# Kernel optimization log

Hardware: AMD Instinct MI355X
Metric: run time of the kernel (lower is better)

Reference implementation:

```python
import jax, jax.numpy as jnp
import numpy as np

H = 1024      # hidden_size
L = 2         # num_layers
V = 32000     # src/tgt vocab
S = 512       # source length
T = 512       # target length
BOS = 0


def _gru_cell(h, x, Wih, Whh, bih, bhh):
    # h,x: [H]; Wih,Whh: [3H,H]; gate order r,z,n (PyTorch convention)
    gi = Wih @ x + bih
    gh = Whh @ h + bhh
    i_r, i_z, i_n = jnp.split(gi, 3)
    h_r, h_z, h_n = jnp.split(gh, 3)
    r = jax.nn.sigmoid(i_r + h_r)
    z = jax.nn.sigmoid(i_z + h_z)
    n = jnp.tanh(i_n + r * h_n)
    return (1.0 - z) * n + z * h


def _run_gru(xs, h0, Wih, Whh, bih, bhh):
    # xs: [T,H] embedded tokens; h0: [L,H]; weights: [L,3H,H]/[L,3H]
    n_layers = Wih.shape[0]

    def step(h, x):
        inp = x
        new_h = []
        for l in range(n_layers):  # small fixed layer loop
            hl = _gru_cell(h[l], inp, Wih[l], Whh[l], bih[l], bhh[l])
            new_h.append(hl)
            inp = hl
        return jnp.stack(new_h), inp  # carry [L,H], emit top-layer hidden

    return jax.lax.scan(step, h0, xs)


def setup_inputs() -> dict:
    key = jax.random.key(0)
    ks = jax.random.split(key, 16)
    sc = 1.0 / np.sqrt(H)

    def gw(k, shape):
        return (jax.random.normal(k, shape, dtype=jnp.float32) * sc)

    return {
        "src_tokens": jax.random.randint(ks[0], (S,), 0, V),
        "tgt_tokens": jax.random.randint(ks[1], (T,), 0, V),
        "src_emb": gw(ks[2], (V, H)),
        "tgt_emb": gw(ks[3], (V, H)),
        "enc_Wih": gw(ks[4], (L, 3 * H, H)),
        "enc_Whh": gw(ks[5], (L, 3 * H, H)),
        "enc_bih": gw(ks[6], (L, 3 * H)),
        "enc_bhh": gw(ks[7], (L, 3 * H)),
        "dec_Wih": gw(ks[8], (L, 3 * H, H)),
        "dec_Whh": gw(ks[9], (L, 3 * H, H)),
        "dec_bih": gw(ks[10], (L, 3 * H)),
        "dec_bhh": gw(ks[11], (L, 3 * H)),
        "out_W": gw(ks[12], (V, H)),
        "out_b": jnp.zeros((V,), dtype=jnp.float32),
    }


def reference(src_tokens, tgt_tokens, src_emb, tgt_emb,
              enc_Wih, enc_Whh, enc_bih, enc_bhh,
              dec_Wih, dec_Whh, dec_bih, dec_bhh,
              out_W, out_b):
    # ---- encoder: embed + L-layer GRU over source ----
    enc_x = src_emb[src_tokens]                       # [S,H]
    h0 = jnp.zeros((enc_Wih.shape[0], src_emb.shape[1]), src_emb.dtype)
    h_enc, _ = _run_gru(enc_x, h0, enc_Wih, enc_Whh, enc_bih, enc_bhh)
    # ---- decoder: teacher-forced inputs [BOS, tgt[:-1]] ----
    dec_in = jnp.concatenate(
        [jnp.array([BOS], dtype=tgt_tokens.dtype), tgt_tokens[:-1]])
    dec_x = tgt_emb[dec_in]                           # [T,H]
    _, dec_top = _run_gru(dec_x, h_enc, dec_Wih, dec_Whh, dec_bih, dec_bhh)
    logits = dec_top @ out_W.T + out_b                # [T,V]
    logp = jax.nn.log_softmax(logits, axis=-1)
    return logp[:, None, None, :]                     # [T,1,1,V] like torch.stack
```

## Files before the change

### kernel.cpp

```cpp
#include <hip/hip_runtime.h>
#include <hip/hip_bf16.h>
#include <math.h>


#define HID 1024
#define NSTEP 512
#define VOCAB 32000
#define SPIN_LIMIT 50000
typedef unsigned long long u64;

__device__ __forceinline__ u64 pack_hv(float v, unsigned tag) {
    return ((u64)tag << 32) | (u64)__float_as_uint(v);
}

__device__ __forceinline__ void poll16(const u64* __restrict__ row, unsigned want,
                                       float* v, int lane) {
    u64 p[16];
    int iter = 0;
    for (;;) {
        bool ok = true;
#pragma unroll
        for (int q = 0; q < 16; ++q) {
            p[q] = __hip_atomic_load((u64*)(row + q * 64 + lane),
                                     __ATOMIC_RELAXED, __HIP_MEMORY_SCOPE_AGENT);
            ok = ok && ((unsigned)(p[q] >> 32) == want);
        }
        if (ok) break;
        if (++iter >= SPIN_LIMIT) {
#pragma unroll
            for (int q = 0; q < 16; ++q) v[q] = __uint_as_float(0x7fc00000u);
            return;
        }
        __builtin_amdgcn_s_sleep(1);
    }
#pragma unroll
    for (int q = 0; q < 16; ++q)
        v[q] = __uint_as_float((unsigned)(p[q] & 0xffffffffu));
}

__global__ __launch_bounds__(256) void gather_embed(
    const int* __restrict__ src_tok, const int* __restrict__ tgt_tok,
    const float* __restrict__ src_emb, const float* __restrict__ tgt_emb,
    float* __restrict__ enc_x, float* __restrict__ dec_x) {
    int b = blockIdx.x, tid = threadIdx.x;
    int tok;
    const float* src;
    float* dst;
    if (b < 512) {
        tok = src_tok[b];
        src = src_emb;
        dst = enc_x + (size_t)b * HID;
    } else {
        int t = b - 512;
        tok = (t == 0) ? 0 : tgt_tok[t - 1];
        src = tgt_emb;
        dst = dec_x + (size_t)t * HID;
    }
    float4 v = *(const float4*)(src + (size_t)tok * HID + tid * 4);
    *(float4*)(dst + tid * 4) = v;
}

__global__ __launch_bounds__(256, 1) void gru_persist(
    const float* __restrict__ enc_x, const float* __restrict__ dec_x,
    const float* __restrict__ eWih, const float* __restrict__ eWhh,
    const float* __restrict__ eBih, const float* __restrict__ eBhh,
    const float* __restrict__ dWih, const float* __restrict__ dWhh,
    const float* __restrict__ dBih, const float* __restrict__ dBhh,
    u64* H0, u64* H1, u64* D0, u64* D1, float* __restrict__ D1f) {
    const int tid = threadIdx.x;
    const int wave = tid >> 6, lane = tid & 63;
    const int role = blockIdx.x >> 7;
    const int wl = blockIdx.x & 127;
    const int j0 = wl * 8;

    __shared__ float dots[48];
    __shared__ float sbias[48];

    float wreg[12][16];
    float hprev = 0.f;

#pragma unroll 1
    for (int phase = 0; phase < 2; ++phase) {
        const bool dec = (phase == 1);
        const float* Wih = (dec ? dWih : eWih) + (size_t)role * 3 * HID * HID;
        const float* Whh = (dec ? dWhh : eWhh) + (size_t)role * 3 * HID * HID;
        const float* bih = (dec ? dBih : eBih) + (size_t)role * 3 * HID;
        const float* bhh = (dec ? dBhh : eBhh) + (size_t)role * 3 * HID;
        u64* hch = dec ? (role ? D1 : D0) : (role ? H1 : H0);
        const unsigned tagOut = dec ? (role ? 4u : 3u) : (role ? 2u : 1u);
        const float* xf = dec ? dec_x : enc_x;
        const u64* xt = dec ? D0 : H0;
        const unsigned tagX = dec ? 3u : 1u;
        const u64* hinit = role ? (H1 + (size_t)(NSTEP - 1) * HID)
                                : (H0 + (size_t)(NSTEP - 1) * HID);
        const unsigned tagInit = role ? 2u : 1u;

        __syncthreads();
#pragma unroll
        for (int r = 0; r < 12; ++r) {
            int R = wave * 12 + r;
            int m = (R < 24) ? R : R - 24;
            const float* base = ((R < 24) ? Wih : Whh) +
                                (size_t)((m >> 3) * HID + j0 + (m & 7)) * HID;
#pragma unroll
            for (int q = 0; q < 16; ++q) wreg[r][q] = base[q * 64 + lane];
        }
        if (tid < 48) {
            int m = (tid < 24) ? tid : tid - 24;
            sbias[tid] = ((tid < 24) ? bih : bhh)[(m >> 3) * HID + j0 + (m & 7)];
        }
        __syncthreads();

#pragma unroll 1
        for (int t = 0; t < NSTEP; ++t) {
            float v[16];
            if (wave < 2) {
                if (role == 0) {
                    const float* xr = xf + (size_t)t * HID;
#pragma unroll
                    for (int q = 0; q < 16; ++q) v[q] = xr[q * 64 + lane];
                } else {
                    poll16(xt + (size_t)t * HID, tagX, v, lane);
                }
            } else {
                if (t > 0) {
                    poll16(hch + (size_t)(t - 1) * HID, tagOut, v, lane);
                } else if (dec) {
                    poll16(hinit, tagInit, v, lane);
                } else {
#pragma unroll
                    for (int q = 0; q < 16; ++q) v[q] = 0.f;
                }
            }

            float part[12];
#pragma unroll
            for (int r = 0; r < 12; ++r) {
                float a = 0.f;
#pragma unroll
                for (int q = 0; q < 16; ++q) a = fmaf(wreg[r][q], v[q], a);
                part[r] = a;
            }
#pragma unroll
            for (int off = 1; off < 64; off <<= 1) {
#pragma unroll
                for (int r = 0; r < 12; ++r) part[r] += __shfl_xor(part[r], off);
            }
            if (lane == 0) {
#pragma unroll
                for (int r = 0; r < 12; ++r) dots[wave * 12 + r] = part[r];
            }
            __syncthreads();

            if (tid < 8) {
                const int jj = tid;
                float ir = dots[jj] + sbias[jj];
                float iz = dots[8 + jj] + sbias[8 + jj];
                float in_ = dots[16 + jj] + sbias[16 + jj];
                float hr = dots[24 + jj] + sbias[24 + jj];
                float hz = dots[32 + jj] + sbias[32 + jj];
                float hn = dots[40 + jj] + sbias[40 + jj];
                float rg = 1.f / (1.f + __expf(-(ir + hr)));
                float zg = 1.f / (1.f + __expf(-(iz + hz)));
                float na = in_ + rg * hn;
                float ng = 2.f / (1.f + __expf(-2.f * na)) - 1.f;
                float hnew = (1.f - zg) * ng + zg * hprev;
                hprev = hnew;
                __hip_atomic_store((u64*)(hch + (size_t)t * HID + j0 + jj),
                                   pack_hv(hnew, tagOut),
                                   __ATOMIC_RELAXED, __HIP_MEMORY_SCOPE_AGENT);
                if (dec && role == 1) D1f[(size_t)t * HID + j0 + jj] = hnew;
            }
            __syncthreads();
        }
    }
}

__global__ __launch_bounds__(256) void gemm_out(
    const float* __restrict__ A, const float* __restrict__ B,
    const float* __restrict__ bias, float* __restrict__ C) {
    const int tid = threadIdx.x;
    const int bi = blockIdx.x;
    const int bv = blockIdx.y;
    const int i0 = bi * 64, v0 = bv * 128;
    __shared__ __align__(16) float As[32 * 68];
    __shared__ __align__(16) float Bs[32 * 132];
    const int tr = tid >> 4, tc = tid & 15;
    float c[4][8] = {};

    for (int kk = 0; kk < HID; kk += 32) {
#pragma unroll
        for (int q = 0; q < 2; q++) {
            int id = tid * 2 + q;
            int r = id >> 3, kq = id & 7;
            float4 a = *(const float4*)&A[(size_t)(i0 + r) * HID + kk + kq * 4];
            As[(kq * 4 + 0) * 68 + r] = a.x;
            As[(kq * 4 + 1) * 68 + r] = a.y;
            As[(kq * 4 + 2) * 68 + r] = a.z;
            As[(kq * 4 + 3) * 68 + r] = a.w;
        }
#pragma unroll
        for (int q = 0; q < 4; q++) {
            int id = tid * 4 + q;
            int vr = id >> 3, kq = id & 7;
            float4 b = *(const float4*)&B[(size_t)(v0 + vr) * HID + kk + kq * 4];
            Bs[(kq * 4 + 0) * 132 + vr] = b.x;
            Bs[(kq * 4 + 1) * 132 + vr] = b.y;
            Bs[(kq * 4 + 2) * 132 + vr] = b.z;
            Bs[(kq * 4 + 3) * 132 + vr] = b.w;
        }
        __syncthreads();
#pragma unroll
        for (int k = 0; k < 32; k++) {
            float4 a4 = *(const float4*)&As[k * 68 + tr * 4];
            float4 b0 = *(const float4*)&Bs[k * 132 + tc * 8];
            float4 b1 = *(const float4*)&Bs[k * 132 + tc * 8 + 4];
            float av[4] = {a4.x, a4.y, a4.z, a4.w};
            float bvv[8] = {b0.x, b0.y, b0.z, b0.w, b1.x, b1.y, b1.z, b1.w};
#pragma unroll
            for (int u = 0; u < 4; u++)
#pragma unroll
                for (int w = 0; w < 8; w++) c[u][w] += av[u] * bvv[w];
        }
        __syncthreads();
    }
    float4 bb0 = *(const float4*)&bias[v0 + tc * 8];
    float4 bb1 = *(const float4*)&bias[v0 + tc * 8 + 4];
#pragma unroll
    for (int u = 0; u < 4; u++) {
        int i = i0 + tr * 4 + u;
        float4 o0 = {c[u][0] + bb0.x, c[u][1] + bb0.y, c[u][2] + bb0.z, c[u][3] + bb0.w};
        float4 o1 = {c[u][4] + bb1.x, c[u][5] + bb1.y, c[u][6] + bb1.z, c[u][7] + bb1.w};
        *(float4*)&C[(size_t)i * VOCAB + v0 + tc * 8] = o0;
        *(float4*)&C[(size_t)i * VOCAB + v0 + tc * 8 + 4] = o1;
    }
}

__global__ __launch_bounds__(256) void log_softmax_inplace(float* __restrict__ C) {
    const int row = blockIdx.x;
    const int tid = threadIdx.x;
    float* p = C + (size_t)row * VOCAB;
    float m = -3.4e38f, s = 0.f;
    for (int idx = tid; idx < VOCAB / 4; idx += 256) {
        float4 x = ((const float4*)p)[idx];
        float xv[4] = {x.x, x.y, x.z, x.w};
#pragma unroll
        for (int u = 0; u < 4; u++) {
            float nm = fmaxf(m, xv[u]);
            s = s * __expf(m - nm) + __expf(xv[u] - nm);
            m = nm;
        }
    }
#pragma unroll
    for (int off = 1; off < 64; off <<= 1) {
        float om = __shfl_xor(m, off);
        float os = __shfl_xor(s, off);
        float nm = fmaxf(m, om);
        s = s * __expf(m - nm) + os * __expf(om - nm);
        m = nm;
    }
    __shared__ float sm[4], ss[4], sL;
    int wv = tid >> 6;
    if ((tid & 63) == 0) { sm[wv] = m; ss[wv] = s; }
    __syncthreads();
    if (tid == 0) {
        float M = sm[0], S = ss[0];
        for (int w = 1; w < 4; w++) {
            float nm = fmaxf(M, sm[w]);
            S = S * __expf(M - nm) + ss[w] * __expf(sm[w] - nm);
            M = nm;
        }
        sL = M + logf(S);
    }
    __syncthreads();
    float L = sL;
    for (int idx = tid; idx < VOCAB / 4; idx += 256) {
        float4 x = ((const float4*)p)[idx];
        x.x -= L; x.y -= L; x.z -= L; x.w -= L;
        ((float4*)p)[idx] = x;
    }
}

extern "C" void kernel_launch(void* const* d_in, const int* in_sizes, int n_in,
                              void* d_out, int out_size, void* d_ws, size_t ws_size,
                              hipStream_t stream) {
    const int* src_tok = (const int*)d_in[0];
    const int* tgt_tok = (const int*)d_in[1];
    const float* src_emb = (const float*)d_in[2];
    const float* tgt_emb = (const float*)d_in[3];
    const float* eWih = (const float*)d_in[4];
    const float* eWhh = (const float*)d_in[5];
    const float* eBih = (const float*)d_in[6];
    const float* eBhh = (const float*)d_in[7];
    const float* dWih = (const float*)d_in[8];
    const float* dWhh = (const float*)d_in[9];
    const float* dBih = (const float*)d_in[10];
    const float* dBhh = (const float*)d_in[11];
    const float* out_W = (const float*)d_in[12];
    const float* out_b = (const float*)d_in[13];
    float* out = (float*)d_out;

    char* ws = (char*)d_ws;
    float* enc_x = (float*)(ws);
    float* dec_x = (float*)(ws + (2ull << 20));
    u64* H0 = (u64*)(ws + (4ull << 20));
    u64* H1 = (u64*)(ws + (8ull << 20));
    u64* D0 = (u64*)(ws + (12ull << 20));
    u64* D1 = (u64*)(ws + (16ull << 20));
    float* D1f = (float*)(ws + (20ull << 20));

    hipMemsetAsync(ws + (4ull << 20), 0, 16ull << 20, stream);

    gather_embed<<<1024, 256, 0, stream>>>(src_tok, tgt_tok, src_emb, tgt_emb, enc_x, dec_x);
    gru_persist<<<256, 256, 0, stream>>>(enc_x, dec_x, eWih, eWhh, eBih, eBhh,
                                         dWih, dWhh, dBih, dBhh, H0, H1, D0, D1, D1f);
    gemm_out<<<dim3(8, 250), 256, 0, stream>>>(D1f, out_W, out_b, out);
    log_softmax_inplace<<<512, 256, 0, stream>>>(out);
}
```

Before: 3.733 ms.

## Run output projection as bf16 MFMA GEMM with per-call weight cast

Adds a kernel that casts the output projection weights to bf16 each call, has the GRU also emit bf16 top-layer hidden states, and replaces the fp32 SIMT output GEMM with a bf16 MFMA GEMM (16x16x32) that loads operands straight from global memory. The goal is to cut the cost of the 512x32000x1024 projection by using matrix cores. In exchange it adds a cast pass over the 32000x1024 weights on every call and lowers the logits to bf16 input precision. The fast path runs only when the workspace holds at least 87 MB; otherwise it falls back to the old fp32 kernel.

```diff
diff --git a/kernel.cpp b/kernel.cpp
--- a/kernel.cpp
+++ b/kernel.cpp
@@ -8,12 +8,17 @@
 #define VOCAB 32000
 #define SPIN_LIMIT 50000
 typedef unsigned long long u64;
-
-__device__ __forceinline__ u64 pack_hv(float v, unsigned tag) {
+typedef unsigned int u32;
+
+__device__ __forceinline__ u64 pack_hv(float v, u32 tag) {
     return ((u64)tag << 32) | (u64)__float_as_uint(v);
 }
-
-__device__ __forceinline__ void poll16(const u64* __restrict__ row, unsigned want,
+__device__ __forceinline__ u32 bf16_rtne(float f) {
+    u32 x = __float_as_uint(f);
+    return (x + 0x7fffu + ((x >> 16) & 1u)) >> 16;
+}
+
+__device__ __forceinline__ void poll16(const u64* __restrict__ row, u32 want,
                                        float* v, int lane) {
     u64 p[16];
     int iter = 0;
@@ -23,7 +28,7 @@
         for (int q = 0; q < 16; ++q) {
             p[q] = __hip_atomic_load((u64*)(row + q * 64 + lane),
                                      __ATOMIC_RELAXED, __HIP_MEMORY_SCOPE_AGENT);
-            ok = ok && ((unsigned)(p[q] >> 32) == want);
+            ok = ok && ((u32)(p[q] >> 32) == want);
         }
         if (ok) break;
         if (++iter >= SPIN_LIMIT) {
@@ -35,7 +40,7 @@
     }
 #pragma unroll
     for (int q = 0; q < 16; ++q)
-        v[q] = __uint_as_float((unsigned)(p[q] & 0xffffffffu));
+        v[q] = __uint_as_float((u32)(p[q] & 0xffffffffu));
 }
 
 __global__ __launch_bounds__(256) void gather_embed(
@@ -60,13 +65,27 @@
     *(float4*)(dst + tid * 4) = v;
 }
 
+__global__ __launch_bounds__(256) void cast_w(const float* __restrict__ W,
+                                              unsigned short* __restrict__ Wb) {
+    size_t base = ((size_t)blockIdx.x * 256 + threadIdx.x) * 8;
+    const float4* s = (const float4*)(W + base);
+    float4 f0 = s[0], f1 = s[1];
+    uint4 o;
+    o.x = bf16_rtne(f0.x) | (bf16_rtne(f0.y) << 16);
+    o.y = bf16_rtne(f0.z) | (bf16_rtne(f0.w) << 16);
+    o.z = bf16_rtne(f1.x) | (bf16_rtne(f1.y) << 16);
+    o.w = bf16_rtne(f1.z) | (bf16_rtne(f1.w) << 16);
+    *(uint4*)(Wb + base) = o;
+}
+
 __global__ __launch_bounds__(256, 1) void gru_persist(
     const float* __restrict__ enc_x, const float* __restrict__ dec_x,
     const float* __restrict__ eWih, const float* __restrict__ eWhh,
     const float* __restrict__ eBih, const float* __restrict__ eBhh,
     const float* __restrict__ dWih, const float* __restrict__ dWhh,
     const float* __restrict__ dBih, const float* __restrict__ dBhh,
-    u64* H0, u64* H1, u64* D0, u64* D1, float* __restrict__ D1f) {
+    u64* H0, u64* H1, u64* D0, u64* D1, float* __restrict__ D1f,
+    unsigned short* __restrict__ D1b) {
     const int tid = threadIdx.x;
     const int wave = tid >> 6, lane = tid & 63;
     const int role = blockIdx.x >> 7;
@@ -87,13 +106,13 @@
         const float* bih = (dec ? dBih : eBih) + (size_t)role * 3 * HID;
         const float* bhh = (dec ? dBhh : eBhh) + (size_t)role * 3 * HID;
         u64* hch = dec ? (role ? D1 : D0) : (role ? H1 : H0);
-        const unsigned tagOut = dec ? (role ? 4u : 3u) : (role ? 2u : 1u);
+        const u32 tagOut = dec ? (role ? 4u : 3u) : (role ? 2u : 1u);
         const float* xf = dec ? dec_x : enc_x;
         const u64* xt = dec ? D0 : H0;
-        const unsigned tagX = dec ? 3u : 1u;
+        const u32 tagX = dec ? 3u : 1u;
         const u64* hinit = role ? (H1 + (size_t)(NSTEP - 1) * HID)
                                 : (H0 + (size_t)(NSTEP - 1) * HID);
-        const unsigned tagInit = role ? 2u : 1u;
+        const u32 tagInit = role ? 2u : 1u;
 
         __syncthreads();
 #pragma unroll
@@ -169,16 +188,61 @@
                 __hip_atomic_store((u64*)(hch + (size_t)t * HID + j0 + jj),
                                    pack_hv(hnew, tagOut),
                                    __ATOMIC_RELAXED, __HIP_MEMORY_SCOPE_AGENT);
-                if (dec && role == 1) D1f[(size_t)t * HID + j0 + jj] = hnew;
+                if (dec && role == 1) {
+                    D1f[(size_t)t * HID + j0 + jj] = hnew;
+                    D1b[(size_t)t * HID + j0 + jj] = (unsigned short)bf16_rtne(hnew);
+                }
             }
             __syncthreads();
         }
+    }
+}
+
+__global__ __launch_bounds__(256) void gemm_mfma(
+    const unsigned short* __restrict__ A, const unsigned short* __restrict__ B,
+    const float* __restrict__ bias, float* __restrict__ C) {
+    typedef __attribute__((ext_vector_type(8))) short short8;
+    typedef __attribute__((ext_vector_type(4))) float f32x4;
+    const int lane = threadIdx.x & 63, wave = threadIdx.x >> 6;
+    const int i0 = blockIdx.x * 64;
+    const int v0 = blockIdx.y * 256 + wave * 64;
+    const int r16 = lane & 15, kq = lane >> 4;
+
+    f32x4 acc[4][4] = {};
+#pragma unroll 4
+    for (int k0 = 0; k0 < HID; k0 += 32) {
+        short8 a[4], b[4];
+#pragma unroll
+        for (int mf = 0; mf < 4; ++mf)
+            a[mf] = *(const short8*)(A + (size_t)(i0 + mf * 16 + r16) * HID + k0 +
+                                     kq * 8);
+#pragma unroll
+        for (int nf = 0; nf < 4; ++nf)
+            b[nf] = *(const short8*)(B + (size_t)(v0 + nf * 16 + r16) * HID + k0 +
+                                     kq * 8);
+#pragma unroll
+        for (int mf = 0; mf < 4; ++mf)
+#pragma unroll
+            for (int nf = 0; nf < 4; ++nf)
+                acc[mf][nf] = __builtin_amdgcn_mfma_f32_16x16x32_bf16(
+                    a[mf], b[nf], acc[mf][nf], 0, 0, 0);
+    }
+#pragma unroll
+    for (int nf = 0; nf < 4; ++nf) {
+        float bb = bias[v0 + nf * 16 + r16];
+#pragma unroll
+        for (int mf = 0; mf < 4; ++mf)
+#pragma unroll
+            for (int reg = 0; reg < 4; ++reg) {
+                int i = i0 + mf * 16 + kq * 4 + reg;
+                C[(size_t)i * VOCAB + v0 + nf * 16 + r16] = acc[mf][nf][reg] + bb;
+            }
     }
 }
 
 __global__ __launch_bounds__(256) void gemm_out(
     const float* __restrict__ A, const float* __restrict__ B,
-    const float* __restrict__ bias, float* __restrict__ C) {
+    const float* __restrict__ bias, float* __restrict__ C, int ldc) {
     const int tid = threadIdx.x;
     const int bi = blockIdx.x;
     const int bv = blockIdx.y;
@@ -231,8 +295,8 @@
         int i = i0 + tr * 4 + u;
         float4 o0 = {c[u][0] + bb0.x, c[u][1] + bb0.y, c[u][2] + bb0.z, c[u][3] + bb0.w};
         float4 o1 = {c[u][4] + bb1.x, c[u][5] + bb1.y, c[u][6] + bb1.z, c[u][7] + bb1.w};
-        *(float4*)&C[(size_t)i * VOCAB + v0 + tc * 8] = o0;
-        *(float4*)&C[(size_t)i * VOCAB + v0 + tc * 8 + 4] = o1;
+        *(float4*)&C[(size_t)i * ldc + v0 + tc * 8] = o0;
+        *(float4*)&C[(size_t)i * ldc + v0 + tc * 8 + 4] = o1;
     }
 }
 
@@ -308,12 +372,23 @@
     u64* D0 = (u64*)(ws + (12ull << 20));
     u64* D1 = (u64*)(ws + (16ull << 20));
     float* D1f = (float*)(ws + (20ull << 20));
+    unsigned short* D1b = (unsigned short*)(ws + (22ull << 20));
+    unsigned short* Wb = (unsigned short*)(ws + (23ull << 20));
+    const bool fast = ws_size >= (87ull << 20);
 
     hipMemsetAsync(ws + (4ull << 20), 0, 16ull << 20, stream);
 
-    gather_embed<<<1024, 256, 0, stream>>>(src_tok, tgt_tok, src_emb, tgt_emb, enc_x, dec_x);
+    gather_embed<<<1024, 256, 0, stream>>>(src_tok, tgt_tok, src_emb, tgt_emb,
+                                           enc_x, dec_x);
+    if (fast) cast_w<<<16000, 256, 0, stream>>>(out_W, Wb);
+
     gru_persist<<<256, 256, 0, stream>>>(enc_x, dec_x, eWih, eWhh, eBih, eBhh,
-                                         dWih, dWhh, dBih, dBhh, H0, H1, D0, D1, D1f);
-    gemm_out<<<dim3(8, 250), 256, 0, stream>>>(D1f, out_W, out_b, out);
+                                         dWih, dWhh, dBih, dBhh, H0, H1, D0, D1,
+                                         D1f, D1b);
+
+    if (fast)
+        gemm_mfma<<<dim3(8, 125), 256, 0, stream>>>(D1b, Wb, out_b, out);
+    else
+        gemm_out<<<dim3(8, 250), 256, 0, stream>>>(D1f, out_W, out_b, out, VOCAB);
     log_softmax_inplace<<<512, 256, 0, stream>>>(out);
 }
```

New measurement: 3.487 ms. -6.6%, faster.
